# Kernel optimization log

Hardware: AMD Instinct MI355X
Metric: run time of the kernel (lower is better)

The kernel has to match this reference:

```python
import jax, jax.numpy as jnp
import numpy as np
from jax import lax

DN = ('NHWC', 'HWIO', 'NHWC')


def _conv(x, w, b=None, stride=1):
    y = lax.conv_general_dilated(x, w, (stride, stride), 'SAME', dimension_numbers=DN)
    return y + b if b is not None else y


def _conv_t(x, w, b, stride=2):
    y = lax.conv_transpose(x, w, (stride, stride), 'SAME', dimension_numbers=DN)
    return y + b


def _res_stack(x, blocks):
    # ResidualBlock: x + Conv1x1(relu(Conv3x3(relu(x)))); final relu after stack
    for w1, w2 in blocks:
        t = jax.nn.relu(x)
        t = _conv(t, w1)          # 3x3, no bias
        t = jax.nn.relu(t)
        t = _conv(t, w2)          # 1x1, no bias
        x = x + t
    return jax.nn.relu(x)


def setup_inputs() -> dict:
    key = jax.random.key(0)
    ks = jax.random.split(key, 32)
    s = 0.05
    n = lambda i, shape: jax.random.normal(ks[i], shape, dtype=jnp.float32) * s
    H, RH, D, K = 128, 32, 128, 512
    return {
        'x': jax.random.normal(ks[0], (16, 256, 256, 3), dtype=jnp.float32),
        'emb': jax.random.normal(ks[1], (K, D), dtype=jnp.float32),  # stddev 1.0 init
        'enc_w1': n(2, (4, 4, 3, H // 2)),  'enc_b1': jnp.zeros((H // 2,), jnp.float32),
        'enc_w2': n(3, (4, 4, H // 2, H)),  'enc_b2': jnp.zeros((H,), jnp.float32),
        'enc_w3': n(4, (3, 3, H, H)),       'enc_b3': jnp.zeros((H,), jnp.float32),
        'erb1_w1': n(5, (3, 3, H, RH)), 'erb1_w2': n(6, (1, 1, RH, H)),
        'erb2_w1': n(7, (3, 3, H, RH)), 'erb2_w2': n(8, (1, 1, RH, H)),
        'dec_w': n(9, (3, 3, D, H)),        'dec_b': jnp.zeros((H,), jnp.float32),
        'drb1_w1': n(10, (3, 3, H, RH)), 'drb1_w2': n(11, (1, 1, RH, H)),
        'drb2_w1': n(12, (3, 3, H, RH)), 'drb2_w2': n(13, (1, 1, RH, H)),
        'dt1_w': n(14, (4, 4, H, H // 2)),  'dt1_b': jnp.zeros((H // 2,), jnp.float32),
        'dt2_w': n(15, (4, 4, H // 2, 3)),  'dt2_b': jnp.zeros((3,), jnp.float32),
    }


def _forward(x, emb, enc_w1, enc_b1, enc_w2, enc_b2, enc_w3, enc_b3,
             erb1_w1, erb1_w2, erb2_w1, erb2_w2,
             dec_w, dec_b, drb1_w1, drb1_w2, drb2_w1, drb2_w2,
             dt1_w, dt1_b, dt2_w, dt2_b):
    f = jax.nn.relu(_conv(x, enc_w1, enc_b1, 2))
    f = jax.nn.relu(_conv(f, enc_w2, enc_b2, 2))
    f = _conv(f, enc_w3, enc_b3, 1)
    f = _res_stack(f, [(erb1_w1, erb1_w2), (erb2_w1, erb2_w2)])
    # VQ: full [N, K] squared-distance matrix, argmin, codebook gather
    D = emb.shape[1]
    flat = f.reshape(-1, D)                                   # [N, D]
    dist = ((flat ** 2).sum(axis=1, keepdims=True)
            + (emb ** 2).sum(axis=1)[None, :]
            - 2.0 * flat @ emb.T)                              # [N, K]
    idx = jnp.argmin(dist, axis=1)                             # [N]
    q = emb[idx].reshape(f.shape)                              # quantized
    y = _conv(q, dec_w, dec_b, 1)
    y = _res_stack(y, [(drb1_w1, drb1_w2), (drb2_w1, drb2_w2)])
    y = jax.nn.relu(_conv_t(y, dt1_w, dt1_b))
    y = _conv_t(y, dt2_w, dt2_b)
    return (y, f, q)


def reference(x, emb, enc_w1, enc_b1, enc_w2, enc_b2, enc_w3, enc_b3,
              erb1_w1, erb1_w2, erb2_w1, erb2_w2,
              dec_w, dec_b, drb1_w1, drb1_w2, drb2_w1, drb2_w2,
              dt1_w, dt1_b, dt2_w, dt2_b):
    return _forward(x, emb, enc_w1, enc_b1, enc_w2, enc_b2, enc_w3, enc_b3,
                    erb1_w1, erb1_w2, erb2_w1, erb2_w2,
                    dec_w, dec_b, drb1_w1, drb1_w2, drb2_w1, drb2_w2,
                    dt1_w, dt1_b, dt2_w, dt2_b)
```

## Files before the change

### kernel.cpp

```cpp
#include <hip/hip_runtime.h>
#include <hip/hip_bf16.h>
#include <hip/hip_fp16.h>

using bf16 = __hip_bfloat16;
using frag_ab = __attribute__((ext_vector_type(8))) short;
using f16x8  = __attribute__((ext_vector_type(8))) _Float16;
using frag_cd = __attribute__((ext_vector_type(4))) float;

enum { F_INRELU = 1, F_OUTRELU = 2, F_RES = 4 };

struct TapSet { int dy[16]; int dx[16]; int wi[16]; };

__device__ __forceinline__ unsigned int relu_pk(unsigned int v) {
    unsigned int m = ((v & 0x80008000u) >> 15) * 0xFFFFu;
    return v & ~m;
}
__device__ __forceinline__ unsigned int mask_by(unsigned int v, unsigned int h) {
    unsigned int m = ((h & 0x80008000u) >> 15) * 0xFFFFu;
    return v & ~m;
}

__global__ void pack_w_k(const float* __restrict__ w, bf16* __restrict__ dst,
                         int Ci, int Co, int BN, TapSet taps, int total)
{
    int idx = blockIdx.x * 256 + threadIdx.x;
    if (idx >= total) return;
    int j  = idx & 7;
    int r1 = idx >> 3;
    int nl = r1 % BN;
    int r2 = r1 / BN;
    int q  = r2 & 3;
    int cb = r2 >> 2;
    int nblocks = Co / BN;
    int c  = cb / nblocks;
    int nb = cb - c * nblocks;
    int cpt = Ci >> 5;
    int tap = c / cpt;
    int ci  = (c - tap * cpt) * 32 + q * 8 + j;
    int n   = nb * BN + nl;
    dst[idx] = __float2bfloat16(w[(size_t)(taps.wi[tap] * Ci + ci) * Co + n]);
}

__global__ void pack_w2_k(const float* __restrict__ w, __half* __restrict__ dst,
                          int Ci, int Co, int BN, TapSet taps, int total)
{
    int idx = blockIdx.x * 256 + threadIdx.x;
    if (idx >= total) return;
    int j  = idx & 7;
    int r1 = idx >> 3;
    int nl = r1 % BN;
    int r2 = r1 / BN;
    int q  = r2 & 3;
    int cb = r2 >> 2;
    int nblocks = Co / BN;
    int c  = cb / nblocks;
    int nb = cb - c * nblocks;
    int cpt = Ci >> 5;
    int tap = c / cpt;
    int ci  = (c - tap * cpt) * 32 + q * 8 + j;
    int n   = nb * BN + nl;
    float v = w[(size_t)(taps.wi[tap] * Ci + ci) * Co + n];
    __half h = __float2half(v);
    __half l = __float2half((v - __half2float(h)) * 2048.0f);
    size_t base = (size_t)cb * (BN * 64) + (q * BN + nl) * 8 + j;
    dst[base] = h;
    dst[base + BN * 32] = l;
}

__global__ void pack_we1_k(const float* __restrict__ w, __half* __restrict__ dst)
{
    int idx = blockIdx.x * 256 + threadIdx.x;
    if (idx >= 4096) return;
    int j  = idx & 7;
    int r1 = idx >> 3;
    int nl = r1 & 63;
    int r2 = r1 >> 6;
    int q  = r2 & 3;
    int c  = r2 >> 2;
    int k  = c * 32 + q * 8 + j;
    int tap = k >> 2, ci = k & 3;
    float v = (ci < 3) ? w[(size_t)(tap * 3 + ci) * 64 + nl] : 0.f;
    __half h = __float2half(v);
    __half l = __float2half((v - __half2float(h)) * 2048.0f);
    size_t base = (size_t)c * 4096 + (q * 64 + nl) * 8 + j;
    dst[base] = h;
    dst[base + 2048] = l;
}

__global__ __launch_bounds__(256) void pad_x_k(
    const float* __restrict__ x, __half* __restrict__ xh, __half* __restrict__ xl)
{
    int pix = blockIdx.x * 256 + threadIdx.x;
    const float* ip = x + (size_t)pix * 3;
    float v0 = ip[0], v1 = ip[1], v2 = ip[2];
    unsigned short hb[4], lb[4];
    float vv[4] = {v0, v1, v2, 0.f};
#pragma unroll
    for (int i = 0; i < 4; ++i) {
        __half h = __float2half(vv[i]);
        hb[i] = __half_as_ushort(h);
        lb[i] = __half_as_ushort(__float2half((vv[i] - __half2float(h)) * 2048.0f));
    }
    uint2 hv = make_uint2((unsigned)hb[0] | ((unsigned)hb[1] << 16),
                          (unsigned)hb[2] | ((unsigned)hb[3] << 16));
    uint2 lv = make_uint2((unsigned)lb[0] | ((unsigned)lb[1] << 16),
                          (unsigned)lb[2] | ((unsigned)lb[3] << 16));
    *(uint2*)(xh + (size_t)pix * 4) = hv;
    *(uint2*)(xl + (size_t)pix * 4) = lv;
}

__global__ __launch_bounds__(256) void enc1_mfma_k(
    const __half* __restrict__ xh, const __half* __restrict__ xl,
    const __half* __restrict__ wp, const float* __restrict__ bias,
    __half* __restrict__ oh, __half* __restrict__ ol)
{
    __shared__ __align__(16) short Ash[64 * 32];
    __shared__ __align__(16) short Asl[64 * 32];
    __shared__ __align__(16) short Bsh[64 * 32];
    __shared__ __align__(16) short Bsl[64 * 32];

    const int tid = threadIdx.x;
    const int m0 = blockIdx.x * 64;

    const int am = tid >> 2;
    const int aq = tid & 3;
    const int gm  = m0 + am;
    const int nn_ = gm >> 14;
    const int rr_ = gm & 16383;
    const int iy0 = (rr_ >> 7) * 2 - 1;
    const int ix0 = (rr_ & 127) * 2 - 1;

    const int lane = tid & 63;
    const int wv4 = tid >> 6;
    const int wm = (wv4 & 1) * 32;
    const int wn = (wv4 >> 1) * 32;
    const int lm = lane & 15, lq = lane >> 4;

    frag_cd accA[2][2], accB[2][2];
#pragma unroll
    for (int i = 0; i < 2; ++i)
#pragma unroll
        for (int j = 0; j < 2; ++j)
#pragma unroll
            for (int r = 0; r < 4; ++r) { accA[i][j][r] = 0.f; accB[i][j][r] = 0.f; }

#pragma unroll
    for (int c = 0; c < 2; ++c) {
        const int tap = c * 8 + aq * 2;
        const int ky = tap >> 2, kx = tap & 3;
        const int iy = iy0 + ky;
        const int ix = ix0 + kx;
        uint2 h0 = make_uint2(0u, 0u), h1 = h0, l0 = h0, l1 = h0;
        if (iy >= 0 && iy < 256) {
            const size_t rowb = (size_t)(nn_ * 256 + iy) * 256;
            if (ix >= 0 && ix < 256) {
                h0 = *(const uint2*)(xh + (rowb + ix) * 4);
                l0 = *(const uint2*)(xl + (rowb + ix) * 4);
            }
            if (ix + 1 >= 0 && ix + 1 < 256) {
                h1 = *(const uint2*)(xh + (rowb + ix + 1) * 4);
                l1 = *(const uint2*)(xl + (rowb + ix + 1) * 4);
            }
        }
        __syncthreads();
        *(uint4*)&Ash[(aq * 64 + am) * 8] = make_uint4(h0.x, h0.y, h1.x, h1.y);
        *(uint4*)&Asl[(aq * 64 + am) * 8] = make_uint4(l0.x, l0.y, l1.x, l1.y);
        {
            const __half* wc = wp + (size_t)c * 4096;
            *(uint4*)&Bsh[tid * 8] = *(const uint4*)(wc + tid * 8);
            *(uint4*)&Bsl[tid * 8] = *(const uint4*)(wc + 2048 + tid * 8);
        }
        __syncthreads();

        f16x8 afh[2], afl[2], bfh[2], bfl[2];
#pragma unroll
        for (int i = 0; i < 2; ++i) {
            afh[i] = *(const f16x8*)&Ash[(lq * 64 + wm + i * 16 + lm) * 8];
            afl[i] = *(const f16x8*)&Asl[(lq * 64 + wm + i * 16 + lm) * 8];
        }
#pragma unroll
        for (int j = 0; j < 2; ++j) {
            bfh[j] = *(const f16x8*)&Bsh[(lq * 64 + wn + j * 16 + lm) * 8];
            bfl[j] = *(const f16x8*)&Bsl[(lq * 64 + wn + j * 16 + lm) * 8];
        }
#pragma unroll
        for (int i = 0; i < 2; ++i)
#pragma unroll
            for (int j = 0; j < 2; ++j) {
                accA[i][j] = __builtin_amdgcn_mfma_f32_16x16x32_f16(afh[i], bfh[j], accA[i][j], 0, 0, 0);
                accB[i][j] = __builtin_amdgcn_mfma_f32_16x16x32_f16(afh[i], bfl[j], accB[i][j], 0, 0, 0);
                accB[i][j] = __builtin_amdgcn_mfma_f32_16x16x32_f16(afl[i], bfh[j], accB[i][j], 0, 0, 0);
            }
    }

    const float s = 1.0f / 2048.0f;
#pragma unroll
    for (int j = 0; j < 2; ++j) {
        const int n_g = wn + j * 16 + lm;
        const float bv = bias[n_g];
#pragma unroll
        for (int i = 0; i < 2; ++i) {
#pragma unroll
            for (int r = 0; r < 4; ++r) {
                const int m_g = m0 + wm + i * 16 + lq * 4 + r;
                const size_t ob = (size_t)m_g * 64 + n_g;
                float v = accA[i][j][r] + accB[i][j][r] * s + bv;
                v = fmaxf(v, 0.f);
                __half h = __float2half(v);
                oh[ob] = h;
                ol[ob] = __float2half((v - __half2float(h)) * 2048.0f);
            }
        }
    }
}

template<int BN>
__global__ __launch_bounds__(256) void conv_mfma2_k(
    const __half* __restrict__ ah, const __half* __restrict__ al,
    const __half* __restrict__ wp, const float* __restrict__ bias,
    float* __restrict__ out, __half* __restrict__ oh, __half* __restrict__ ol,
    const __half* __restrict__ rh, const __half* __restrict__ rl,
    int IH, int IW, int Ci, int Co, int sy_in,
    TapSet taps, int ntaps, int flags)
{
    __shared__ __align__(16) short Ash[64 * 32];
    __shared__ __align__(16) short Asl[64 * 32];
    __shared__ __align__(16) short Bsh[BN * 32];
    __shared__ __align__(16) short Bsl[BN * 32];

    const int tid = threadIdx.x;
    const int m0 = blockIdx.x * 64;
    const int n0 = blockIdx.y * BN;

    const int am = tid >> 2;
    const int aq = tid & 3;
    const int gm  = m0 + am;
    const int nn_ = gm >> 12;
    const int rr_ = gm & 4095;
    const int oy_ = (rr_ >> 6) * sy_in;
    const int ox_ = (rr_ & 63) * sy_in;

    const int lane = tid & 63;
    const int wv4 = tid >> 6;
    constexpr int MT = (BN == 64) ? 2 : 1;
    constexpr int NT = 2;
    const int wm = (BN == 64) ? (wv4 & 1) * 32 : wv4 * 16;
    const int wn = (BN == 64) ? (wv4 >> 1) * 32 : 0;
    const int lm = lane & 15, lq = lane >> 4;
    constexpr int NLOAD = BN * 32 / 8;

    frag_cd accA[MT][NT], accB[MT][NT];
#pragma unroll
    for (int i = 0; i < MT; ++i)
#pragma unroll
        for (int j = 0; j < NT; ++j)
#pragma unroll
            for (int r = 0; r < 4; ++r) { accA[i][j][r] = 0.f; accB[i][j][r] = 0.f; }

    const int cpt = Ci >> 5;
    const int nch = ntaps * cpt;
    const bool inrelu = (flags & F_INRELU) != 0;

    int tap = 0, cc = 0, ci0 = 0;
    for (int c = 0; c < nch; ++c) {
        const int iy = oy_ + taps.dy[tap];
        const int ix = ox_ + taps.dx[tap];
        uint4 avh = make_uint4(0u, 0u, 0u, 0u);
        uint4 avl = make_uint4(0u, 0u, 0u, 0u);
        if (iy >= 0 && iy < IH && ix >= 0 && ix < IW) {
            const size_t off = (size_t)((nn_ * IH + iy) * IW + ix) * Ci + ci0 + aq * 8;
            avh = *(const uint4*)(ah + off);
            avl = *(const uint4*)(al + off);
        }
        if (inrelu) {
            avl.x = mask_by(avl.x, avh.x); avl.y = mask_by(avl.y, avh.y);
            avl.z = mask_by(avl.z, avh.z); avl.w = mask_by(avl.w, avh.w);
            avh.x = relu_pk(avh.x); avh.y = relu_pk(avh.y);
            avh.z = relu_pk(avh.z); avh.w = relu_pk(avh.w);
        }
        uint4 bvh, bvl;
        if (tid < NLOAD) {
            const __half* wc = wp + (size_t)(c * gridDim.y + blockIdx.y) * (BN * 64);
            bvh = *(const uint4*)(wc + tid * 8);
            bvl = *(const uint4*)(wc + BN * 32 + tid * 8);
        }

        __syncthreads();
        *(uint4*)&Ash[(aq * 64 + am) * 8] = avh;
        *(uint4*)&Asl[(aq * 64 + am) * 8] = avl;
        if (tid < NLOAD) {
            *(uint4*)&Bsh[tid * 8] = bvh;
            *(uint4*)&Bsl[tid * 8] = bvl;
        }
        __syncthreads();

        f16x8 afh[MT], afl[MT], bfh[NT], bfl[NT];
#pragma unroll
        for (int i = 0; i < MT; ++i) {
            afh[i] = *(const f16x8*)&Ash[(lq * 64 + wm + i * 16 + lm) * 8];
            afl[i] = *(const f16x8*)&Asl[(lq * 64 + wm + i * 16 + lm) * 8];
        }
#pragma unroll
        for (int j = 0; j < NT; ++j) {
            bfh[j] = *(const f16x8*)&Bsh[(lq * BN + wn + j * 16 + lm) * 8];
            bfl[j] = *(const f16x8*)&Bsl[(lq * BN + wn + j * 16 + lm) * 8];
        }
#pragma unroll
        for (int i = 0; i < MT; ++i)
#pragma unroll
            for (int j = 0; j < NT; ++j) {
                accA[i][j] = __builtin_amdgcn_mfma_f32_16x16x32_f16(afh[i], bfh[j], accA[i][j], 0, 0, 0);
                accB[i][j] = __builtin_amdgcn_mfma_f32_16x16x32_f16(afh[i], bfl[j], accB[i][j], 0, 0, 0);
                accB[i][j] = __builtin_amdgcn_mfma_f32_16x16x32_f16(afl[i], bfh[j], accB[i][j], 0, 0, 0);
            }

        ci0 += 32;
        if (++cc == cpt) { cc = 0; ci0 = 0; ++tap; }
    }

    const float s = 1.0f / 2048.0f;
#pragma unroll
    for (int j = 0; j < NT; ++j) {
        const int n_g = n0 + wn + j * 16 + lm;
        const float bv = bias ? bias[n_g] : 0.f;
#pragma unroll
        for (int i = 0; i < MT; ++i) {
#pragma unroll
            for (int r = 0; r < 4; ++r) {
                const int m_g = m0 + wm + i * 16 + lq * 4 + r;
                const size_t ob = (size_t)m_g * Co + n_g;
                float v = accA[i][j][r] + accB[i][j][r] * s + bv;
                if (flags & F_RES)
                    v += __half2float(rh[ob]) + __half2float(rl[ob]) * s;
                if (flags & F_OUTRELU) v = fmaxf(v, 0.f);
                if (out) out[ob] = v;
                if (oh) {
                    __half h = __float2half(v);
                    oh[ob] = h;
                    ol[ob] = __float2half((v - __half2float(h)) * 2048.0f);
                }
            }
        }
    }
}

template<int BN>
__global__ __launch_bounds__(256) void conv_mfma_k(
    const bf16* __restrict__ a, const bf16* __restrict__ wp,
    const float* __restrict__ bias,
    float* __restrict__ out, bf16* __restrict__ out_bf,
    const float* __restrict__ res,
    int Ci, int Co, int OHf, int OWf, int sy_out, int py, int px,
    TapSet taps, int ntaps, int flags)
{
    __shared__ __align__(16) short As[64 * 32];
    __shared__ __align__(16) short Bs[BN * 32];

    const int tid = threadIdx.x;
    const int m0 = blockIdx.x * 64;
    const int n0 = blockIdx.y * BN;

    const int am = tid >> 2;
    const int aq = tid & 3;
    const int gm  = m0 + am;
    const int nn_ = gm >> 12;
    const int rr_ = gm & 4095;
    const int oy_ = rr_ >> 6;
    const int ox_ = rr_ & 63;

    const int lane = tid & 63;
    const int wv4 = tid >> 6;
    constexpr int MT = (BN == 64) ? 2 : 1;
    constexpr int NT = 2;
    const int wm = (BN == 64) ? (wv4 & 1) * 32 : wv4 * 16;
    const int wn = (BN == 64) ? (wv4 >> 1) * 32 : 0;
    const int lm = lane & 15, lq = lane >> 4;
    constexpr int NLOAD = BN * 32 / 8;

    frag_cd acc[MT][NT];
#pragma unroll
    for (int i = 0; i < MT; ++i)
#pragma unroll
        for (int j = 0; j < NT; ++j)
#pragma unroll
            for (int r = 0; r < 4; ++r) acc[i][j][r] = 0.f;

    const int cpt = Ci >> 5;
    const int nch = ntaps * cpt;
    const bool inrelu = (flags & F_INRELU) != 0;

    int tap = 0, cc = 0, ci0 = 0;
    for (int c = 0; c < nch; ++c) {
        const int iy = oy_ + taps.dy[tap];
        const int ix = ox_ + taps.dx[tap];
        uint4 av = make_uint4(0u, 0u, 0u, 0u);
        if (iy >= 0 && iy < 64 && ix >= 0 && ix < 64)
            av = *(const uint4*)(a + (size_t)((nn_ * 64 + iy) * 64 + ix) * Ci + ci0 + aq * 8);
        if (inrelu) {
            av.x = relu_pk(av.x); av.y = relu_pk(av.y);
            av.z = relu_pk(av.z); av.w = relu_pk(av.w);
        }
        uint4 bv;
        if (tid < NLOAD)
            bv = *(const uint4*)(wp + ((size_t)c * gridDim.y + blockIdx.y) * (BN * 32) + tid * 8);

        __syncthreads();
        *(uint4*)&As[(aq * 64 + am) * 8] = av;
        if (tid < NLOAD) *(uint4*)&Bs[tid * 8] = bv;
        __syncthreads();

        frag_ab af[MT], bfr[NT];
#pragma unroll
        for (int i = 0; i < MT; ++i)
            af[i] = *(const frag_ab*)&As[(lq * 64 + wm + i * 16 + lm) * 8];
#pragma unroll
        for (int j = 0; j < NT; ++j)
            bfr[j] = *(const frag_ab*)&Bs[(lq * BN + wn + j * 16 + lm) * 8];
#pragma unroll
        for (int i = 0; i < MT; ++i)
#pragma unroll
            for (int j = 0; j < NT; ++j)
                acc[i][j] = __builtin_amdgcn_mfma_f32_16x16x32_bf16(af[i], bfr[j], acc[i][j], 0, 0, 0);

        ci0 += 32;
        if (++cc == cpt) { cc = 0; ci0 = 0; ++tap; }
    }

#pragma unroll
    for (int j = 0; j < NT; ++j) {
        const int n_g = n0 + wn + j * 16 + lm;
        const float bv = bias ? bias[n_g] : 0.f;
#pragma unroll
        for (int i = 0; i < MT; ++i) {
#pragma unroll
            for (int r = 0; r < 4; ++r) {
                const int m_g = m0 + wm + i * 16 + lq * 4 + r;
                const int nn2 = m_g >> 12;
                const int rr2 = m_g & 4095;
                const int oy = (rr2 >> 6) * sy_out + py;
                const int ox = (rr2 & 63) * sy_out + px;
                const size_t ob = ((size_t)(nn2 * OHf + oy) * OWf + ox) * Co + n_g;
                float v = acc[i][j][r] + bv;
                if (flags & F_RES)     v += res[ob];
                if (flags & F_OUTRELU) v = fmaxf(v, 0.f);
                if (out)    out[ob]    = v;
                if (out_bf) out_bf[ob] = __float2bfloat16(v);
            }
        }
    }
}

__global__ __launch_bounds__(256) void convt_final_k(
    const float* __restrict__ in, const float* __restrict__ w,
    const float* __restrict__ bias, float* __restrict__ out)
{
    __shared__ __align__(16) float Wl[1536];
    const int tid = threadIdx.x;
    const int row = blockIdx.x;
    const int n   = row >> 8;
    const int oy  = row & 255;
    const int pY  = oy & 1;
    for (int i = tid; i < 1536; i += 256) {
        int co  = i >> 9;
        int rem = i & 511;
        int tap = rem >> 6;
        int ci  = rem & 63;
        int ky  = pY + ((tap >> 2) << 1);
        int kx  = tap & 3;
        Wl[i] = w[(size_t)((ky * 4 + kx) * 64 + ci) * 3 + co];
    }
    __syncthreads();
    const int wv = tid >> 6;
    const int p  = wv & 1;
    const int m  = ((wv >> 1) << 6) + (tid & 63);
    const int ox = 2 * m + p;
    float a0a = bias[0], a1a = bias[1], a2a = bias[2];
    float a0b = 0.f, a1b = 0.f, a2b = 0.f;
#pragma unroll
    for (int kyi = 0; kyi < 2; ++kyi) {
        int iy2 = oy + pY + 2 * kyi - 2;
        if (iy2 < 0 || iy2 >= 256) continue;
        int iy = iy2 >> 1;
#pragma unroll
        for (int t = 0; t < 2; ++t) {
            int ix = m + p + t - 1;
            if (ix < 0 || ix >= 128) continue;
            const float* ip = in + (size_t)((n * 128 + iy) * 128 + ix) * 64;
            const int kx = p + 2 * t;
            const float* w0 = Wl + ((kyi * 4 + kx) << 6);
            const float* w1 = w0 + 512;
            const float* w2 = w1 + 512;
#pragma unroll
            for (int q = 0; q < 16; ++q) {
                float4 v  = *(const float4*)(ip + q * 4);
                float4 b0 = *(const float4*)(w0 + q * 4);
                float4 b1 = *(const float4*)(w1 + q * 4);
                float4 b2 = *(const float4*)(w2 + q * 4);
                a0a = fmaf(v.x, b0.x, a0a); a0b = fmaf(v.y, b0.y, a0b);
                a0a = fmaf(v.z, b0.z, a0a); a0b = fmaf(v.w, b0.w, a0b);
                a1a = fmaf(v.x, b1.x, a1a); a1b = fmaf(v.y, b1.y, a1b);
                a1a = fmaf(v.z, b1.z, a1a); a1b = fmaf(v.w, b1.w, a1b);
                a2a = fmaf(v.x, b2.x, a2a); a2b = fmaf(v.y, b2.y, a2b);
                a2a = fmaf(v.z, b2.z, a2a); a2b = fmaf(v.w, b2.w, a2b);
            }
        }
    }
    float* op = out + (size_t)((n * 256 + oy) * 256 + ox) * 3;
    op[0] = a0a + a0b;
    op[1] = a1a + a1b;
    op[2] = a2a + a2b;
}

__global__ void enorm_k(const float* __restrict__ emb, float* __restrict__ en) {
    int k = blockIdx.x * 256 + threadIdx.x;
    if (k >= 512) return;
    const float4* e = (const float4*)(emb + k * 128);
    float s = 0.f;
    for (int i = 0; i < 32; ++i) {
        float4 v = e[i];
        s += v.x * v.x + v.y * v.y + v.z * v.z + v.w * v.w;
    }
    en[k] = s;
}

__global__ void pack_emb_k(const float* __restrict__ emb, __half* __restrict__ dst)
{
    int idx = blockIdx.x * 256 + threadIdx.x;
    int k = idx & 127;
    int n = idx >> 7;
    float v = emb[idx];
    __half h = __float2half(v);
    __half l = __float2half((v - __half2float(h)) * 2048.0f);
    int nb = n >> 6, nl = n & 63;
    int ch = k >> 5, q = (k >> 3) & 3, j = k & 7;
    size_t base = (size_t)(nb * 4 + ch) * 4096 + (q * 64 + nl) * 8 + j;
    dst[base] = h;
    dst[base + 2048] = l;
}

__global__ __launch_bounds__(256) void vq_mfma_k(
    const __half* __restrict__ fh, const __half* __restrict__ fl,
    const __half* __restrict__ pe, const float* __restrict__ en,
    const float* __restrict__ emb, float* __restrict__ q, bf16* __restrict__ qb)
{
    __shared__ __align__(16) short Ash[64 * 128];
    __shared__ __align__(16) short Asl[64 * 128];
    __shared__ int sel[64];

    const int tid  = threadIdx.x;
    const int pos0 = blockIdx.x * 64;

    {
        const int am = tid >> 2;
        const int aq = tid & 3;
#pragma unroll
        for (int ch = 0; ch < 4; ++ch) {
            const size_t off = (size_t)(pos0 + am) * 128 + ch * 32 + aq * 8;
            uint4 vh = *(const uint4*)(fh + off);
            uint4 vl = *(const uint4*)(fl + off);
            *(uint4*)&Ash[((ch * 4 + aq) * 64 + am) * 8] = vh;
            *(uint4*)&Asl[((ch * 4 + aq) * 64 + am) * 8] = vl;
        }
    }
    __syncthreads();

    const int lane = tid & 63;
    const int w    = tid >> 6;
    const int lm = lane & 15, lq = lane >> 4;
    const int mbase = w * 16;
    const float s = 1.0f / 2048.0f;

    float best[4] = {3.4e38f, 3.4e38f, 3.4e38f, 3.4e38f};
    int   bidx[4] = {0, 0, 0, 0};

    f16x8 ah[4], alv[4];
#pragma unroll
    for (int ch = 0; ch < 4; ++ch) {
        ah[ch]  = *(const f16x8*)&Ash[((ch * 4 + lq) * 64 + mbase + lm) * 8];
        alv[ch] = *(const f16x8*)&Asl[((ch * 4 + lq) * 64 + mbase + lm) * 8];
    }

    for (int nb = 0; nb < 8; ++nb) {
        frag_cd accA[4], accB[4];
#pragma unroll
        for (int j = 0; j < 4; ++j)
#pragma unroll
            for (int r = 0; r < 4; ++r) { accA[j][r] = 0.f; accB[j][r] = 0.f; }

#pragma unroll
        for (int ch = 0; ch < 4; ++ch) {
            const __half* base = pe + (size_t)(nb * 4 + ch) * 4096;
            f16x8 bh[4], bl[4];
#pragma unroll
            for (int j = 0; j < 4; ++j) {
                const int o = (lq * 64 + j * 16 + lm) * 8;
                bh[j] = *(const f16x8*)(base + o);
                bl[j] = *(const f16x8*)(base + 2048 + o);
            }
#pragma unroll
            for (int j = 0; j < 4; ++j) {
                accA[j] = __builtin_amdgcn_mfma_f32_16x16x32_f16(ah[ch], bh[j], accA[j], 0, 0, 0);
                accB[j] = __builtin_amdgcn_mfma_f32_16x16x32_f16(ah[ch], bl[j], accB[j], 0, 0, 0);
                accB[j] = __builtin_amdgcn_mfma_f32_16x16x32_f16(alv[ch], bh[j], accB[j], 0, 0, 0);
            }
        }

#pragma unroll
        for (int j = 0; j < 4; ++j) {
            const int code = nb * 64 + j * 16 + lm;
            const float ec = en[code];
#pragma unroll
            for (int r = 0; r < 4; ++r) {
                float dot = accA[j][r] + accB[j][r] * s;
                float d = fmaf(dot, -2.f, ec);
                if (d < best[r]) { best[r] = d; bidx[r] = code; }
            }
        }
    }

#pragma unroll
    for (int r = 0; r < 4; ++r) {
        float d = best[r]; int ix = bidx[r];
#pragma unroll
        for (int m = 1; m < 16; m <<= 1) {
            float d2 = __shfl_xor(d, m);
            int   x2 = __shfl_xor(ix, m);
            if (d2 < d || (d2 == d && x2 < ix)) { d = d2; ix = x2; }
        }
        if (lm == 0) sel[mbase + lq * 4 + r] = ix;
    }
    __syncthreads();

#pragma unroll
    for (int jj = 0; jj < 32; ++jj) {
        int id = jj * 256 + tid;
        int p = id >> 7, k = id & 127;
        float v = emb[(size_t)sel[p] * 128 + k];
        q[(size_t)(pos0 + p) * 128 + k]  = v;
        qb[(size_t)(pos0 + p) * 128 + k] = __float2bfloat16(v);
    }
}

static TapSet conv_taps(int KH, int KW, int pad) {
    TapSet t{};
    for (int ky = 0; ky < KH; ++ky)
        for (int kx = 0; kx < KW; ++kx) {
            int i = ky * KW + kx;
            t.dy[i] = ky - pad; t.dx[i] = kx - pad; t.wi[i] = i;
        }
    return t;
}

static TapSet convt_taps(int py, int px) {
    TapSet t{};
    for (int ty = 0; ty < 2; ++ty)
        for (int tx = 0; tx < 2; ++tx) {
            int i = ty * 2 + tx;
            t.dy[i] = py + ty - 1;
            t.dx[i] = px + tx - 1;
            t.wi[i] = (py + 2 * ty) * 4 + (px + 2 * tx);
        }
    return t;
}

extern "C" void kernel_launch(void* const* d_in, const int* in_sizes, int n_in,
                              void* d_out, int out_size, void* d_ws, size_t ws_size,
                              hipStream_t stream)
{
    const float* x       = (const float*)d_in[0];
    const float* emb     = (const float*)d_in[1];
    const float* enc_w1  = (const float*)d_in[2];
    const float* enc_b1  = (const float*)d_in[3];
    const float* enc_w2  = (const float*)d_in[4];
    const float* enc_b2  = (const float*)d_in[5];
    const float* enc_w3  = (const float*)d_in[6];
    const float* enc_b3  = (const float*)d_in[7];
    const float* erb1_w1 = (const float*)d_in[8];
    const float* erb1_w2 = (const float*)d_in[9];
    const float* erb2_w1 = (const float*)d_in[10];
    const float* erb2_w2 = (const float*)d_in[11];
    const float* dec_w   = (const float*)d_in[12];
    const float* dec_b   = (const float*)d_in[13];
    const float* drb1_w1 = (const float*)d_in[14];
    const float* drb1_w2 = (const float*)d_in[15];
    const float* drb2_w1 = (const float*)d_in[16];
    const float* drb2_w2 = (const float*)d_in[17];
    const float* dt1_w   = (const float*)d_in[18];
    const float* dt1_b   = (const float*)d_in[19];
    const float* dt2_w   = (const float*)d_in[20];
    const float* dt2_b   = (const float*)d_in[21];

    char* wsb = (char*)d_ws;
    __half* H1 = (__half*)wsb;
    __half* L1 = (__half*)(wsb + (size_t)33554432);
    __half* H2 = (__half*)(wsb + (size_t)67108864);
    __half* L2 = (__half*)(wsb + (size_t)83886080);
    __half* Xh = (__half*)(wsb + (size_t)67108864);
    __half* Xl = (__half*)(wsb + (size_t)75497472);
    __half* H3 = (__half*)wsb;
    __half* L3 = (__half*)(wsb + (size_t)16777216);
    __half* H4 = (__half*)(wsb + (size_t)33554432);
    __half* L4 = (__half*)(wsb + (size_t)50331648);
    __half* Ht = (__half*)(wsb + (size_t)100663296);
    __half* Lt = (__half*)(wsb + (size_t)104857600);
    float*  EN = (float*)(wsb + (size_t)109051904);
    __half* Fh = (__half*)wsb;
    __half* Fl = (__half*)(wsb + (size_t)16777216);
    bf16* Qb  = (bf16*)(wsb + (size_t)67108864);
    bf16* Db  = (bf16*)(wsb + (size_t)83886080);
    bf16* Y1b = Qb;
    bf16* Y2b = Db;
    bf16* Tb  = (bf16*)(wsb + (size_t)100663296);
    float* Y0 = (float*)wsb;
    float* Y1 = (float*)(wsb + (size_t)33554432);
    float* A1 = (float*)wsb;
    char* pk = wsb + (size_t)109056000;
    bf16* Pdec  = (bf16*)pk;  pk += 147456 * 2;
    bf16* Pd1w1 = (bf16*)pk;  pk += 36864 * 2;
    bf16* Pd1w2 = (bf16*)pk;  pk += 4096 * 2;
    bf16* Pd2w1 = (bf16*)pk;  pk += 36864 * 2;
    bf16* Pd2w2 = (bf16*)pk;  pk += 4096 * 2;
    bf16* Pdt1[4];
    for (int i = 0; i < 4; ++i) { Pdt1[i] = (bf16*)pk; pk += 65536 * 2; }
    __half* P2enc2 = (__half*)pk; pk += 131072 * 4;
    __half* P2enc3 = (__half*)pk; pk += 147456 * 4;
    __half* P2e1w1 = (__half*)pk; pk += 36864 * 4;
    __half* P2e1w2 = (__half*)pk; pk += 4096 * 4;
    __half* P2e2w1 = (__half*)pk; pk += 36864 * 4;
    __half* P2e2w2 = (__half*)pk; pk += 4096 * 4;
    __half* Pe     = (__half*)pk; pk += 131072 * 2;
    __half* Pe1    = (__half*)pk; pk += 8192 * 2;

    float* outY = (float*)d_out;
    float* outF = outY + 3145728;
    float* outQ = outF + 8388608;

    const TapSet t3 = conv_taps(3, 3, 1);
    const TapSet t4 = conv_taps(4, 4, 1);
    const TapSet t1 = conv_taps(1, 1, 0);
    TapSet tdt[4];
    for (int p = 0; p < 4; ++p) tdt[p] = convt_taps(p >> 1, p & 1);

    enorm_k<<<2, 256, 0, stream>>>(emb, EN);
    pack_emb_k<<<256, 256, 0, stream>>>(emb, Pe);
    pack_we1_k<<<16, 256, 0, stream>>>(enc_w1, Pe1);

    pack_w_k<<<(147456 + 255) / 256, 256, 0, stream>>>(dec_w, Pdec, 128, 128, 64, t3, 147456);
    pack_w_k<<<(36864 + 255) / 256, 256, 0, stream>>>(drb1_w1, Pd1w1, 128, 32, 32, t3, 36864);
    pack_w_k<<<(4096 + 255) / 256, 256, 0, stream>>>(drb1_w2, Pd1w2, 32, 128, 64, t1, 4096);
    pack_w_k<<<(36864 + 255) / 256, 256, 0, stream>>>(drb2_w1, Pd2w1, 128, 32, 32, t3, 36864);
    pack_w_k<<<(4096 + 255) / 256, 256, 0, stream>>>(drb2_w2, Pd2w2, 32, 128, 64, t1, 4096);
    for (int p = 0; p < 4; ++p)
        pack_w_k<<<(65536 + 255) / 256, 256, 0, stream>>>(dt1_w, Pdt1[p], 128, 64, 64, tdt[p], 65536);
    pack_w2_k<<<(131072 + 255) / 256, 256, 0, stream>>>(enc_w2, P2enc2, 64, 128, 64, t4, 131072);
    pack_w2_k<<<(147456 + 255) / 256, 256, 0, stream>>>(enc_w3, P2enc3, 128, 128, 64, t3, 147456);
    pack_w2_k<<<(36864 + 255) / 256, 256, 0, stream>>>(erb1_w1, P2e1w1, 128, 32, 32, t3, 36864);
    pack_w2_k<<<(4096 + 255) / 256, 256, 0, stream>>>(erb1_w2, P2e1w2, 32, 128, 64, t1, 4096);
    pack_w2_k<<<(36864 + 255) / 256, 256, 0, stream>>>(erb2_w1, P2e2w1, 128, 32, 32, t3, 36864);
    pack_w2_k<<<(4096 + 255) / 256, 256, 0, stream>>>(erb2_w2, P2e2w2, 32, 128, 64, t1, 4096);

    pad_x_k<<<4096, 256, 0, stream>>>(x, Xh, Xl);
    enc1_mfma_k<<<4096, 256, 0, stream>>>(Xh, Xl, Pe1, enc_b1, H1, L1);
    conv_mfma2_k<64><<<dim3(1024, 2), 256, 0, stream>>>(H1, L1, P2enc2, enc_b2,
        nullptr, H2, L2, nullptr, nullptr, 128, 128, 64, 128, 2, t4, 16, F_OUTRELU);
    conv_mfma2_k<64><<<dim3(1024, 2), 256, 0, stream>>>(H2, L2, P2enc3, enc_b3,
        nullptr, H3, L3, nullptr, nullptr, 64, 64, 128, 128, 1, t3, 9, 0);
    conv_mfma2_k<32><<<dim3(1024, 1), 256, 0, stream>>>(H3, L3, P2e1w1, nullptr,
        nullptr, Ht, Lt, nullptr, nullptr, 64, 64, 128, 32, 1, t3, 9, F_INRELU);
    conv_mfma2_k<64><<<dim3(1024, 2), 256, 0, stream>>>(Ht, Lt, P2e1w2, nullptr,
        nullptr, H4, L4, H3, L3, 64, 64, 32, 128, 1, t1, 1, F_INRELU | F_RES);
    conv_mfma2_k<32><<<dim3(1024, 1), 256, 0, stream>>>(H4, L4, P2e2w1, nullptr,
        nullptr, Ht, Lt, nullptr, nullptr, 64, 64, 128, 32, 1, t3, 9, F_INRELU);
    conv_mfma2_k<64><<<dim3(1024, 2), 256, 0, stream>>>(Ht, Lt, P2e2w2, nullptr,
        outF, Fh, Fl, H4, L4, 64, 64, 32, 128, 1, t1, 1, F_INRELU | F_RES | F_OUTRELU);

    vq_mfma_k<<<1024, 256, 0, stream>>>(Fh, Fl, Pe, EN, emb, outQ, Qb);

    conv_mfma_k<64><<<dim3(1024, 2), 256, 0, stream>>>(Qb, Pdec, dec_b, Y0, Db, nullptr,
        128, 128, 64, 64, 1, 0, 0, t3, 9, 0);
    conv_mfma_k<32><<<dim3(1024, 1), 256, 0, stream>>>(Db, Pd1w1, nullptr, nullptr, Tb, nullptr,
        128, 32, 64, 64, 1, 0, 0, t3, 9, F_INRELU);
    conv_mfma_k<64><<<dim3(1024, 2), 256, 0, stream>>>(Tb, Pd1w2, nullptr, Y1, Y1b, Y0,
        32, 128, 64, 64, 1, 0, 0, t1, 1, F_INRELU | F_RES);
    conv_mfma_k<32><<<dim3(1024, 1), 256, 0, stream>>>(Y1b, Pd2w1, nullptr, nullptr, Tb, nullptr,
        128, 32, 64, 64, 1, 0, 0, t3, 9, F_INRELU);
    conv_mfma_k<64><<<dim3(1024, 2), 256, 0, stream>>>(Tb, Pd2w2, nullptr, nullptr, Y2b, Y1,
        32, 128, 64, 64, 1, 0, 0, t1, 1, F_INRELU | F_RES | F_OUTRELU);
    for (int p = 0; p < 4; ++p)
        conv_mfma_k<64><<<dim3(1024, 1), 256, 0, stream>>>(Y2b, Pdt1[p], dt1_b, A1, nullptr, nullptr,
            128, 64, 128, 128, 2, p >> 1, p & 1, tdt[p], 4, F_OUTRELU);
    convt_final_k<<<4096, 256, 0, stream>>>(A1, dt2_w, dt2_b, outY);
}
```

Baseline: 916.3 us.

## Compute all four output phases per input pixel in final transposed conv

The final stride-2 transposed conv now assigns one input pixel per thread. Each thread loads its 3x3 neighbourhood of the 64-channel input once and produces the 2x2 block of output pixels, instead of one output pixel per thread re-reading up to 4 input pixels. Out-of-bounds neighbours point at a small zeroed pad buffer, which removes branches. Weights are read directly from global memory (uniform, cached) instead of being staged in shared memory. The trade is more registers per thread (9 float4s plus 12 accumulators) and a quarter as many blocks, which may cut occupancy.

```diff
diff --git a/kernel.cpp b/kernel.cpp
--- a/kernel.cpp
+++ b/kernel.cpp
@@ -87,6 +87,8 @@
     dst[base + 2048] = l;
 }
 
+__global__ void zero64_k(float* __restrict__ z) { z[threadIdx.x] = 0.f; }
+
 __global__ __launch_bounds__(256) void pad_x_k(
     const float* __restrict__ x, __half* __restrict__ xh, __half* __restrict__ xl)
 {
@@ -452,63 +454,71 @@
 
 __global__ __launch_bounds__(256) void convt_final_k(
     const float* __restrict__ in, const float* __restrict__ w,
-    const float* __restrict__ bias, float* __restrict__ out)
-{
-    __shared__ __align__(16) float Wl[1536];
+    const float* __restrict__ bias, const float* __restrict__ zpad,
+    float* __restrict__ out)
+{
     const int tid = threadIdx.x;
-    const int row = blockIdx.x;
-    const int n   = row >> 8;
-    const int oy  = row & 255;
-    const int pY  = oy & 1;
-    for (int i = tid; i < 1536; i += 256) {
-        int co  = i >> 9;
-        int rem = i & 511;
-        int tap = rem >> 6;
-        int ci  = rem & 63;
-        int ky  = pY + ((tap >> 2) << 1);
-        int kx  = tap & 3;
-        Wl[i] = w[(size_t)((ky * 4 + kx) * 64 + ci) * 3 + co];
-    }
-    __syncthreads();
-    const int wv = tid >> 6;
-    const int p  = wv & 1;
-    const int m  = ((wv >> 1) << 6) + (tid & 63);
-    const int ox = 2 * m + p;
-    float a0a = bias[0], a1a = bias[1], a2a = bias[2];
-    float a0b = 0.f, a1b = 0.f, a2b = 0.f;
-#pragma unroll
-    for (int kyi = 0; kyi < 2; ++kyi) {
-        int iy2 = oy + pY + 2 * kyi - 2;
-        if (iy2 < 0 || iy2 >= 256) continue;
-        int iy = iy2 >> 1;
-#pragma unroll
-        for (int t = 0; t < 2; ++t) {
-            int ix = m + p + t - 1;
-            if (ix < 0 || ix >= 128) continue;
-            const float* ip = in + (size_t)((n * 128 + iy) * 128 + ix) * 64;
-            const int kx = p + 2 * t;
-            const float* w0 = Wl + ((kyi * 4 + kx) << 6);
-            const float* w1 = w0 + 512;
-            const float* w2 = w1 + 512;
-#pragma unroll
-            for (int q = 0; q < 16; ++q) {
-                float4 v  = *(const float4*)(ip + q * 4);
-                float4 b0 = *(const float4*)(w0 + q * 4);
-                float4 b1 = *(const float4*)(w1 + q * 4);
-                float4 b2 = *(const float4*)(w2 + q * 4);
-                a0a = fmaf(v.x, b0.x, a0a); a0b = fmaf(v.y, b0.y, a0b);
-                a0a = fmaf(v.z, b0.z, a0a); a0b = fmaf(v.w, b0.w, a0b);
-                a1a = fmaf(v.x, b1.x, a1a); a1b = fmaf(v.y, b1.y, a1b);
-                a1a = fmaf(v.z, b1.z, a1a); a1b = fmaf(v.w, b1.w, a1b);
-                a2a = fmaf(v.x, b2.x, a2a); a2b = fmaf(v.y, b2.y, a2b);
-                a2a = fmaf(v.z, b2.z, a2a); a2b = fmaf(v.w, b2.w, a2b);
-            }
-        }
-    }
-    float* op = out + (size_t)((n * 256 + oy) * 256 + ox) * 3;
-    op[0] = a0a + a0b;
-    op[1] = a1a + a1b;
-    op[2] = a2a + a2b;
+    const int m   = tid & 127;
+    const int rl  = tid >> 7;
+    const int blk = blockIdx.x;
+    const int n   = blk >> 6;
+    const int R   = ((blk & 63) << 1) + rl;
+
+    const float* p[3][3];
+#pragma unroll
+    for (int i = 0; i < 3; ++i) {
+        const int iy = R - 1 + i;
+        const bool vy = ((unsigned)iy < 128u);
+#pragma unroll
+        for (int j = 0; j < 3; ++j) {
+            const int ix = m - 1 + j;
+            const bool v = vy && ((unsigned)ix < 128u);
+            p[i][j] = v ? (in + (size_t)((n * 128 + iy) * 128 + ix) * 64) : zpad;
+        }
+    }
+
+    float acc[2][2][3];
+#pragma unroll
+    for (int a = 0; a < 2; ++a)
+#pragma unroll
+        for (int b = 0; b < 2; ++b)
+#pragma unroll
+            for (int c = 0; c < 3; ++c) acc[a][b][c] = 0.f;
+
+#pragma unroll 2
+    for (int q = 0; q < 16; ++q) {
+        float4 v[3][3];
+#pragma unroll
+        for (int i = 0; i < 3; ++i)
+#pragma unroll
+            for (int j = 0; j < 3; ++j)
+                v[i][j] = *(const float4*)(p[i][j] + q * 4);
+
+        const float* wq = w + q * 12;
+#pragma unroll
+        for (int ky = 0; ky < 4; ++ky)
+#pragma unroll
+            for (int kx = 0; kx < 4; ++kx) {
+                const float* ww = wq + (ky * 4 + kx) * 192;
+                const float4 u = v[(ky >> 1) + (ky & 1)][(kx >> 1) + (kx & 1)];
+                const int a = ky & 1, b = kx & 1;
+                acc[a][b][0] += u.x * ww[0] + u.y * ww[3] + u.z * ww[6] + u.w * ww[9];
+                acc[a][b][1] += u.x * ww[1] + u.y * ww[4] + u.z * ww[7] + u.w * ww[10];
+                acc[a][b][2] += u.x * ww[2] + u.y * ww[5] + u.z * ww[8] + u.w * ww[11];
+            }
+    }
+
+    const float b0 = bias[0], b1 = bias[1], b2 = bias[2];
+#pragma unroll
+    for (int a = 0; a < 2; ++a) {
+        float* op = out + (size_t)((n * 256 + 2 * R + a) * 256 + 2 * m) * 3;
+        op[0] = acc[a][0][0] + b0;
+        op[1] = acc[a][0][1] + b1;
+        op[2] = acc[a][0][2] + b2;
+        op[3] = acc[a][1][0] + b0;
+        op[4] = acc[a][1][1] + b1;
+        op[5] = acc[a][1][2] + b2;
+    }
 }
 
 __global__ void enorm_k(const float* __restrict__ emb, float* __restrict__ en) {
@@ -704,6 +714,7 @@
     __half* Ht = (__half*)(wsb + (size_t)100663296);
     __half* Lt = (__half*)(wsb + (size_t)104857600);
     float*  EN = (float*)(wsb + (size_t)109051904);
+    float*  Zp = (float*)(wsb + (size_t)109053952);
     __half* Fh = (__half*)wsb;
     __half* Fl = (__half*)(wsb + (size_t)16777216);
     bf16* Qb  = (bf16*)(wsb + (size_t)67108864);
@@ -744,6 +755,7 @@
     enorm_k<<<2, 256, 0, stream>>>(emb, EN);
     pack_emb_k<<<256, 256, 0, stream>>>(emb, Pe);
     pack_we1_k<<<16, 256, 0, stream>>>(enc_w1, Pe1);
+    zero64_k<<<1, 64, 0, stream>>>(Zp);
 
     pack_w_k<<<(147456 + 255) / 256, 256, 0, stream>>>(dec_w, Pdec, 128, 128, 64, t3, 147456);
     pack_w_k<<<(36864 + 255) / 256, 256, 0, stream>>>(drb1_w1, Pd1w1, 128, 32, 32, t3, 36864);
@@ -789,5 +801,5 @@
     for (int p = 0; p < 4; ++p)
         conv_mfma_k<64><<<dim3(1024, 1), 256, 0, stream>>>(Y2b, Pdt1[p], dt1_b, A1, nullptr, nullptr,
             128, 64, 128, 128, 2, p >> 1, p & 1, tdt[p], 4, F_OUTRELU);
-    convt_final_k<<<4096, 256, 0, stream>>>(A1, dt2_w, dt2_b, outY);
-}
+    convt_final_k<<<1024, 256, 0, stream>>>(A1, dt2_w, dt2_b, Zp, outY);
+}
```

After: 1.074 ms. 1.17x slower.

## Replace scalar final transposed conv with split-fp16 MFMA kernel

Applied to the files above, without the earlier changes.

The final 64->3 channel transposed convolution, previously computed with scalar FMAs per output pixel, is rewritten as a per-parity implicit GEMM on MFMA 16x16x32 f16 instructions. Activations are split on the fly into hi/lo fp16 pairs and weights are prepacked (N padded from 3 to 16) so precision stays near fp32. This trades mostly wasted MFMA columns (13 of 16) and extra conversion and LDS sync work for matrix-core throughput. Each block handles only 64 pixels with 8 synchronised K-steps, so per-block overhead may dominate.

```diff
diff --git a/kernel.cpp b/kernel.cpp
--- a/kernel.cpp
+++ b/kernel.cpp
@@ -67,6 +67,33 @@
     dst[base + BN * 32] = l;
 }
 
+__global__ void pack_wdt2_k(const float* __restrict__ w, __half* __restrict__ dst)
+{
+    int idx = blockIdx.x * 256 + threadIdx.x;
+    if (idx >= 16384) return;
+    int parity = idx >> 12;
+    int r0 = idx & 4095;
+    int j  = r0 & 7;
+    int r1 = r0 >> 3;
+    int nl = r1 & 15;
+    int r2 = r1 >> 4;
+    int q  = r2 & 3;
+    int cb = r2 >> 2;
+    int tap = cb >> 1;
+    int cc  = cb & 1;
+    int ci  = cc * 32 + q * 8 + j;
+    int n   = nl;
+    int py = parity >> 1, px = parity & 1;
+    int ty = tap >> 1, tx = tap & 1;
+    int wi = (py + 2 * ty) * 4 + (px + 2 * tx);
+    float v = (n < 3) ? w[(size_t)(wi * 64 + ci) * 3 + n] : 0.f;
+    __half h = __float2half(v);
+    __half l = __float2half((v - __half2float(h)) * 2048.0f);
+    size_t base = (size_t)parity * 8192 + cb * 1024 + (q * 16 + nl) * 8 + j;
+    dst[base] = h;
+    dst[base + 512] = l;
+}
+
 __global__ void pack_we1_k(const float* __restrict__ w, __half* __restrict__ dst)
 {
     int idx = blockIdx.x * 256 + threadIdx.x;
@@ -450,65 +477,107 @@
     }
 }
 
-__global__ __launch_bounds__(256) void convt_final_k(
-    const float* __restrict__ in, const float* __restrict__ w,
-    const float* __restrict__ bias, float* __restrict__ out)
-{
-    __shared__ __align__(16) float Wl[1536];
+__global__ __launch_bounds__(256) void dt2_mfma_k(
+    const float* __restrict__ in,
+    const __half* __restrict__ wp,
+    const float* __restrict__ bias,
+    float* __restrict__ out)
+{
+    __shared__ __align__(16) short Ash[64 * 32];
+    __shared__ __align__(16) short Asl[64 * 32];
+    __shared__ __align__(16) short Bsh[16 * 32];
+    __shared__ __align__(16) short Bsl[16 * 32];
+
     const int tid = threadIdx.x;
-    const int row = blockIdx.x;
-    const int n   = row >> 8;
-    const int oy  = row & 255;
-    const int pY  = oy & 1;
-    for (int i = tid; i < 1536; i += 256) {
-        int co  = i >> 9;
-        int rem = i & 511;
-        int tap = rem >> 6;
-        int ci  = rem & 63;
-        int ky  = pY + ((tap >> 2) << 1);
-        int kx  = tap & 3;
-        Wl[i] = w[(size_t)((ky * 4 + kx) * 64 + ci) * 3 + co];
-    }
-    __syncthreads();
-    const int wv = tid >> 6;
-    const int p  = wv & 1;
-    const int m  = ((wv >> 1) << 6) + (tid & 63);
-    const int ox = 2 * m + p;
-    float a0a = bias[0], a1a = bias[1], a2a = bias[2];
-    float a0b = 0.f, a1b = 0.f, a2b = 0.f;
-#pragma unroll
-    for (int kyi = 0; kyi < 2; ++kyi) {
-        int iy2 = oy + pY + 2 * kyi - 2;
-        if (iy2 < 0 || iy2 >= 256) continue;
-        int iy = iy2 >> 1;
-#pragma unroll
-        for (int t = 0; t < 2; ++t) {
-            int ix = m + p + t - 1;
-            if (ix < 0 || ix >= 128) continue;
-            const float* ip = in + (size_t)((n * 128 + iy) * 128 + ix) * 64;
-            const int kx = p + 2 * t;
-            const float* w0 = Wl + ((kyi * 4 + kx) << 6);
-            const float* w1 = w0 + 512;
-            const float* w2 = w1 + 512;
-#pragma unroll
-            for (int q = 0; q < 16; ++q) {
-                float4 v  = *(const float4*)(ip + q * 4);
-                float4 b0 = *(const float4*)(w0 + q * 4);
-                float4 b1 = *(const float4*)(w1 + q * 4);
-                float4 b2 = *(const float4*)(w2 + q * 4);
-                a0a = fmaf(v.x, b0.x, a0a); a0b = fmaf(v.y, b0.y, a0b);
-                a0a = fmaf(v.z, b0.z, a0a); a0b = fmaf(v.w, b0.w, a0b);
-                a1a = fmaf(v.x, b1.x, a1a); a1b = fmaf(v.y, b1.y, a1b);
-                a1a = fmaf(v.z, b1.z, a1a); a1b = fmaf(v.w, b1.w, a1b);
-                a2a = fmaf(v.x, b2.x, a2a); a2b = fmaf(v.y, b2.y, a2b);
-                a2a = fmaf(v.z, b2.z, a2a); a2b = fmaf(v.w, b2.w, a2b);
-            }
-        }
-    }
-    float* op = out + (size_t)((n * 256 + oy) * 256 + ox) * 3;
-    op[0] = a0a + a0b;
-    op[1] = a1a + a1b;
-    op[2] = a2a + a2b;
+    const int par = blockIdx.x & 3;
+    const int m0  = (blockIdx.x >> 2) * 64;
+    const int py = par >> 1, px = par & 1;
+
+    const int am = tid >> 2;
+    const int aq = tid & 3;
+    const int gm  = m0 + am;
+    const int nn_ = gm >> 14;
+    const int rr_ = gm & 16383;
+    const int r_  = rr_ >> 7;
+    const int c_  = rr_ & 127;
+
+    const int lane = tid & 63;
+    const int wv4 = tid >> 6;
+    const int wm = wv4 * 16;
+    const int lm = lane & 15, lq = lane >> 4;
+
+    frag_cd accA, accB;
+#pragma unroll
+    for (int r = 0; r < 4; ++r) { accA[r] = 0.f; accB[r] = 0.f; }
+
+    const __half* wpar = wp + (size_t)par * 8192;
+
+    for (int c = 0; c < 8; ++c) {
+        const int tap = c >> 1;
+        const int iy = r_ + py + (tap >> 1) - 1;
+        const int ix = c_ + px + (tap & 1) - 1;
+        const int ci0 = (c & 1) * 32;
+        uint4 hi = make_uint4(0u, 0u, 0u, 0u);
+        uint4 lo = make_uint4(0u, 0u, 0u, 0u);
+        if ((unsigned)iy < 128u && (unsigned)ix < 128u) {
+            const float* ip = in + (size_t)((nn_ * 128 + iy) * 128 + ix) * 64 + ci0 + aq * 8;
+            const float4 v0 = *(const float4*)ip;
+            const float4 v1 = *(const float4*)(ip + 4);
+            float vv[8] = {v0.x, v0.y, v0.z, v0.w, v1.x, v1.y, v1.z, v1.w};
+            unsigned short hb[8], lb[8];
+#pragma unroll
+            for (int i = 0; i < 8; ++i) {
+                __half h = __float2half(vv[i]);
+                hb[i] = __half_as_ushort(h);
+                lb[i] = __half_as_ushort(__float2half((vv[i] - __half2float(h)) * 2048.0f));
+            }
+            hi = make_uint4((unsigned)hb[0] | ((unsigned)hb[1] << 16),
+                            (unsigned)hb[2] | ((unsigned)hb[3] << 16),
+                            (unsigned)hb[4] | ((unsigned)hb[5] << 16),
+                            (unsigned)hb[6] | ((unsigned)hb[7] << 16));
+            lo = make_uint4((unsigned)lb[0] | ((unsigned)lb[1] << 16),
+                            (unsigned)lb[2] | ((unsigned)lb[3] << 16),
+                            (unsigned)lb[4] | ((unsigned)lb[5] << 16),
+                            (unsigned)lb[6] | ((unsigned)lb[7] << 16));
+        }
+        uint4 bvh, bvl;
+        if (tid < 64) {
+            const __half* wc = wpar + c * 1024;
+            bvh = *(const uint4*)(wc + tid * 8);
+            bvl = *(const uint4*)(wc + 512 + tid * 8);
+        }
+
+        __syncthreads();
+        *(uint4*)&Ash[(aq * 64 + am) * 8] = hi;
+        *(uint4*)&Asl[(aq * 64 + am) * 8] = lo;
+        if (tid < 64) {
+            *(uint4*)&Bsh[tid * 8] = bvh;
+            *(uint4*)&Bsl[tid * 8] = bvl;
+        }
+        __syncthreads();
+
+        const f16x8 afh = *(const f16x8*)&Ash[(lq * 64 + wm + lm) * 8];
+        const f16x8 afl = *(const f16x8*)&Asl[(lq * 64 + wm + lm) * 8];
+        const f16x8 bfh = *(const f16x8*)&Bsh[(lq * 16 + lm) * 8];
+        const f16x8 bfl = *(const f16x8*)&Bsl[(lq * 16 + lm) * 8];
+        accA = __builtin_amdgcn_mfma_f32_16x16x32_f16(afh, bfh, accA, 0, 0, 0);
+        accB = __builtin_amdgcn_mfma_f32_16x16x32_f16(afh, bfl, accB, 0, 0, 0);
+        accB = __builtin_amdgcn_mfma_f32_16x16x32_f16(afl, bfh, accB, 0, 0, 0);
+    }
+
+    const float s = 1.0f / 2048.0f;
+    if (lm < 3) {
+        const float bv = bias[lm];
+#pragma unroll
+        for (int r = 0; r < 4; ++r) {
+            const int m_g = m0 + wm + lq * 4 + r;
+            const int nn2 = m_g >> 14;
+            const int rr2 = m_g & 16383;
+            const int oy = (rr2 >> 7) * 2 + py;
+            const int ox = (rr2 & 127) * 2 + px;
+            out[((size_t)(nn2 * 256 + oy) * 256 + ox) * 3 + lm] = accA[r] + accB[r] * s + bv;
+        }
+    }
 }
 
 __global__ void enorm_k(const float* __restrict__ emb, float* __restrict__ en) {
@@ -730,6 +799,7 @@
     __half* P2e2w2 = (__half*)pk; pk += 4096 * 4;
     __half* Pe     = (__half*)pk; pk += 131072 * 2;
     __half* Pe1    = (__half*)pk; pk += 8192 * 2;
+    __half* Pdt2   = (__half*)pk; pk += 32768 * 2;
 
     float* outY = (float*)d_out;
     float* outF = outY + 3145728;
@@ -744,6 +814,7 @@
     enorm_k<<<2, 256, 0, stream>>>(emb, EN);
     pack_emb_k<<<256, 256, 0, stream>>>(emb, Pe);
     pack_we1_k<<<16, 256, 0, stream>>>(enc_w1, Pe1);
+    pack_wdt2_k<<<64, 256, 0, stream>>>(dt2_w, Pdt2);
 
     pack_w_k<<<(147456 + 255) / 256, 256, 0, stream>>>(dec_w, Pdec, 128, 128, 64, t3, 147456);
     pack_w_k<<<(36864 + 255) / 256, 256, 0, stream>>>(drb1_w1, Pd1w1, 128, 32, 32, t3, 36864);
@@ -789,5 +860,6 @@
     for (int p = 0; p < 4; ++p)
         conv_mfma_k<64><<<dim3(1024, 1), 256, 0, stream>>>(Y2b, Pdt1[p], dt1_b, A1, nullptr, nullptr,
             128, 64, 128, 128, 2, p >> 1, p & 1, tdt[p], 4, F_OUTRELU);
-    convt_final_k<<<4096, 256, 0, stream>>>(A1, dt2_w, dt2_b, outY);
-}
+
+    dt2_mfma_k<<<16384, 256, 0, stream>>>(A1, Pdt2, dt2_b, outY);
+}
```

Result: faster. 889.4 us (-2.9%).
